# Kernel tuning notes

Measured on AMD Instinct MI355X. Metric: run time of the kernel, lower is better.

## Reference

```python
import jax, jax.numpy as jnp
import numpy as np

B, S, D = 4, 4096, 64

def setup_inputs() -> dict:
    key = jax.random.key(0)
    kq, kk, kv = jax.random.split(key, 3)
    return {
        "q": jax.random.normal(kq, (B, S, D), dtype=jnp.float32),
        "k": jax.random.normal(kk, (B, S, D), dtype=jnp.float32),
        "v": jax.random.normal(kv, (B, S, D), dtype=jnp.float32),
    }

def reference(q, k, v):
    # scores: [B, Sq, Sk]; NOTE: scale is k.shape[-1] (not sqrt), per the source.
    scores = jnp.einsum("bqd,bkd->bqk", q, k) / k.shape[-1]
    # softmax over dim=1 == the QUERY axis (non-standard), then matmul V.
    probs = jax.nn.softmax(scores, axis=1)            # [B, Sq, Sk]
    attn = jnp.einsum("bqk,bkd->bqd", probs, v)       # [B, Sq, D]
    attn_w = jax.nn.softmax(attn, axis=1)             # softmax over Sq again
    return (attn, attn_w)
```

## Files before the change

### kernel.cpp

```cpp
#include <hip/hip_runtime.h>
#include <hip/hip_bf16.h>
#include <math.h>

#define BB 4
#define SS 4096
#define DD 64
#define KSPLIT 4
#define QSPLIT 8

typedef __attribute__((ext_vector_type(8))) short short8;
typedef __attribute__((ext_vector_type(4))) float f32x4;
typedef __attribute__((ext_vector_type(2))) unsigned int u32x2;
typedef unsigned int u32;
typedef unsigned short ushort_t;

#define MFMA16(a,b,c) __builtin_amdgcn_mfma_f32_16x16x32_bf16((a),(b),(c),0,0,0)
#define C2SC 0.022542110700140054f

#define BAR() do { asm volatile("" ::: "memory"); \
                   __builtin_amdgcn_s_barrier();  \
                   asm volatile("" ::: "memory"); } while (0)
#define WAIT_VM(N)  asm volatile("s_waitcnt vmcnt(" #N ")" ::: "memory")
#define WAIT_LGKM() asm volatile("s_waitcnt lgkmcnt(0)" ::: "memory")

union Pk8 { short8 s8; u32 u[4]; u32x2 h[2]; };

static __device__ __forceinline__ unsigned short f2bf(float f) {
  union { float f; u32 u; } x; x.f = f;
  u32 r = (x.u + 0x7FFFu + ((x.u >> 16) & 1u)) >> 16;
  return (unsigned short)r;
}

static __device__ __forceinline__ u32 pk2(float a, float b) {
  __hip_bfloat16 lo = __float2bfloat16(a);
  __hip_bfloat16 hi = __float2bfloat16(b);
  unsigned short ls, hs;
  __builtin_memcpy(&ls, &lo, 2); __builtin_memcpy(&hs, &hi, 2);
  return (u32)ls | ((u32)hs << 16);
}

static __device__ __forceinline__ void gload16(const void* g, void* l) {
  __builtin_amdgcn_global_load_lds((const __attribute__((address_space(1))) u32*)g,
                                   (__attribute__((address_space(3))) u32*)l, 16, 0, 0);
}

__global__ __launch_bounds__(256) void p0_convert(
    const float* __restrict__ q, const float* __restrict__ k,
    ushort_t* __restrict__ QB, ushort_t* __restrict__ KB,
    float* __restrict__ out0, float* __restrict__ z2)
{
  const size_t i = (size_t)blockIdx.x * 256 + threadIdx.x;
  float4 a = ((const float4*)q)[i];
  float4 c = ((const float4*)k)[i];
  ((ushort4*)QB)[i] = make_ushort4(f2bf(a.x), f2bf(a.y), f2bf(a.z), f2bf(a.w));
  ((ushort4*)KB)[i] = make_ushort4(f2bf(c.x), f2bf(c.y), f2bf(c.z), f2bf(c.w));
  ((float4*)out0)[i] = make_float4(0.f, 0.f, 0.f, 0.f);
  if (blockIdx.x == 0) z2[threadIdx.x] = 0.f;
}

__global__ __launch_bounds__(256, 4) void pa_colsum(
    const ushort_t* __restrict__ QB, const ushort_t* __restrict__ KB,
    float* __restrict__ Zp)
{
  const int kb0 = blockIdx.x * 128;
  const int qch = blockIdx.y;
  const int b   = blockIdx.z;
  const int t = threadIdx.x, w = t >> 6, lane = t & 63;
  const int g = lane >> 4, r15 = lane & 15;
  const int QCH = SS / QSPLIT;
  const int NT = QCH / 64;

  __shared__ alignas(16) char qbuf[2][64*128];

  short8 ak[2][2];
#pragma unroll
  for (int s = 0; s < 2; ++s)
#pragma unroll
    for (int dh = 0; dh < 2; ++dh)
      ak[s][dh] = *(const short8*)(KB + ((size_t)b*SS + kb0 + 32*w + 16*s + r15)*DD + 32*dh + 8*g);

  const int q0g = qch * QCH;
#define PA_STAGE(tt, buf) do {                                              \
    _Pragma("unroll")                                                       \
    for (int j = 0; j < 2; ++j) {                                           \
      const int row = 16*w + 8*j + (lane >> 3);                             \
      const char* gsrc = (const char*)(QB + ((size_t)b*SS + q0g + (tt)*64 + row)*DD) \
                         + 16*((lane & 7) ^ (row & 7));                     \
      gload16(gsrc, qbuf[buf] + (16*w + 8*j)*128);                          \
    }                                                                       \
  } while (0)

  PA_STAGE(0, 0);

  float z[8];
#pragma unroll
  for (int i = 0; i < 8; ++i) z[i] = 0.f;

#pragma unroll 1
  for (int tt = 0; tt < NT; ++tt) {
    if (tt < NT-1) {
      PA_STAGE(tt+1, (tt+1)&1);
      WAIT_VM(2);
    } else {
      WAIT_VM(0);
    }
    BAR();
    const char* qb = qbuf[tt & 1];
#pragma unroll
    for (int qt = 0; qt < 4; ++qt) {
      const int qrow = 16*qt + r15;
      const char* base = qb + qrow*128;
      short8 bq0 = *(const short8*)(base + 16*((g    ) ^ (qrow & 7)));
      short8 bq1 = *(const short8*)(base + 16*((4 + g) ^ (qrow & 7)));
#pragma unroll
      for (int s = 0; s < 2; ++s) {
        f32x4 a = {0.f,0.f,0.f,0.f};
        a = MFMA16(ak[s][0], bq0, a);
        a = MFMA16(ak[s][1], bq1, a);
        z[4*s+0] += exp2f(a[0]*C2SC); z[4*s+1] += exp2f(a[1]*C2SC);
        z[4*s+2] += exp2f(a[2]*C2SC); z[4*s+3] += exp2f(a[3]*C2SC);
      }
    }
    WAIT_LGKM();
    BAR();
  }
#undef PA_STAGE

#pragma unroll
  for (int m = 1; m < 16; m <<= 1)
#pragma unroll
    for (int i = 0; i < 8; ++i) z[i] += __shfl_xor(z[i], m);
  if (r15 == 0) {
#pragma unroll
    for (int s = 0; s < 2; ++s)
#pragma unroll
      for (int r = 0; r < 4; ++r)
        Zp[((size_t)qch*BB + b)*SS + kb0 + 32*w + 16*s + 4*g + r] = z[4*s+r];
  }
}

__global__ __launch_bounds__(256) void p2_vt(
    const float* __restrict__ v, const float* __restrict__ Zp,
    ushort_t* __restrict__ VT)
{
  const int k0 = blockIdx.x * 64;
  const int b  = blockIdx.y;
  const int t = threadIdx.x;
  __shared__ float vs[64][65];
  __shared__ float izs[64];
  {
    const int row = t >> 2, cq = (t & 3) * 16;
    const float* src = v + ((size_t)b*SS + k0 + row)*DD + cq;
#pragma unroll
    for (int i = 0; i < 4; ++i) {
      float4 x = ((const float4*)src)[i];
      vs[row][cq + 4*i + 0] = x.x; vs[row][cq + 4*i + 1] = x.y;
      vs[row][cq + 4*i + 2] = x.z; vs[row][cq + 4*i + 3] = x.w;
    }
  }
  if (t < 64) {
    float z = 0.f;
#pragma unroll
    for (int c = 0; c < QSPLIT; ++c)
      z += Zp[((size_t)c*BB + b)*SS + k0 + t];
    izs[t] = 1.0f / z;
  }
  __syncthreads();
  const int d = t >> 2, ks = (t & 3) * 16;
  u32* dst = (u32*)VT + (((size_t)b*DD + d)*SS + k0 + ks)/2;
#pragma unroll
  for (int i = 0; i < 8; ++i) {
    float a0 = vs[ks + 2*i    ][d] * izs[ks + 2*i    ];
    float a1 = vs[ks + 2*i + 1][d] * izs[ks + 2*i + 1];
    dst[i] = (u32)f2bf(a0) | ((u32)f2bf(a1) << 16);
  }
}

__global__ __launch_bounds__(256, 2) void pb_attn(
    const ushort_t* __restrict__ QB, const ushort_t* __restrict__ KB,
    const ushort_t* __restrict__ VT, float* __restrict__ out0)
{
  const int q0 = blockIdx.x * 64;
  const int kbase = blockIdx.y * (SS / KSPLIT);
  const int b  = blockIdx.z;
  const int t = threadIdx.x, w = t >> 6, lane = t & 63;
  const int g = lane >> 4, r15 = lane & 15;
  const int NT = SS / KSPLIT / 128;

  __shared__ alignas(16) char smem[65536];
  char* kbuf = smem;
  char* vbuf = smem + 32768;

  short8 aq[4][2];
#pragma unroll
  for (int qt = 0; qt < 4; ++qt)
#pragma unroll
    for (int dh = 0; dh < 2; ++dh)
      aq[qt][dh] = *(const short8*)(QB + ((size_t)b*SS + q0 + 16*qt + r15)*DD + 32*dh + 8*g);

  f32x4 acc[4][4];
#pragma unroll
  for (int qt = 0; qt < 4; ++qt)
#pragma unroll
    for (int dt = 0; dt < 4; ++dt) acc[qt][dt] = (f32x4){0.f,0.f,0.f,0.f};

#define PB_STAGE(kt, buf) do {                                               \
    const int kc = kbase + (kt)*128;                                         \
    _Pragma("unroll")                                                        \
    for (int j = 0; j < 4; ++j) {                                            \
      const int row = 32*j + 8*w + (lane >> 3);                              \
      const char* gk = (const char*)(KB + ((size_t)b*SS + kc + row)*DD)      \
                       + 16*((lane & 7) ^ (row & 7));                        \
      gload16(gk, kbuf + (buf)*16384 + (32*j + 8*w)*128);                    \
    }                                                                        \
    _Pragma("unroll")                                                        \
    for (int j = 0; j < 4; ++j) {                                            \
      const int row = 16*j + 4*w + (lane >> 4);                              \
      const char* gv = (const char*)(VT + ((size_t)b*DD + row)*SS + kc)      \
                       + 16*((lane & 15) ^ (row & 15));                      \
      gload16(gv, vbuf + (buf)*16384 + (16*j + 4*w)*256);                    \
    }                                                                        \
  } while (0)

  PB_STAGE(0, 0);

#pragma unroll 1
  for (int kt = 0; kt < NT; ++kt) {
    if (kt < NT-1) {
      PB_STAGE(kt+1, (kt+1)&1);
      WAIT_VM(8);
    } else {
      WAIT_VM(0);
    }
    BAR();
    const char* kb = kbuf + (kt&1)*16384;
    const char* vb = vbuf + (kt&1)*16384;

    u32 pk[2][4][2];
#pragma unroll
    for (int s = 0; s < 2; ++s) {
      const int rowA = 64*s + 16*w + r15;
      const char* base = kb + rowA*128;
      short8 ka0 = *(const short8*)(base + 16*((g    ) ^ (rowA & 7)));
      short8 ka1 = *(const short8*)(base + 16*((4 + g) ^ (rowA & 7)));
#pragma unroll
      for (int qt = 0; qt < 4; ++qt) {
        f32x4 a = {0.f,0.f,0.f,0.f};
        a = MFMA16(ka0, aq[qt][0], a);
        a = MFMA16(ka1, aq[qt][1], a);
        pk[s][qt][0] = pk2(exp2f(a[0]*C2SC), exp2f(a[1]*C2SC));
        pk[s][qt][1] = pk2(exp2f(a[2]*C2SC), exp2f(a[3]*C2SC));
      }
    }
    short8 bv[4];
#pragma unroll
    for (int dt = 0; dt < 4; ++dt) {
      const int vrow = 16*dt + r15;
      Pk8 u;
      u.h[0] = *(const u32x2*)(vb + vrow*256 + 16*((    2*w + (g>>1)) ^ r15) + 8*(g&1));
      u.h[1] = *(const u32x2*)(vb + vrow*256 + 16*((8 + 2*w + (g>>1)) ^ r15) + 8*(g&1));
      bv[dt] = u.s8;
    }
#pragma unroll
    for (int qt = 0; qt < 4; ++qt) {
      Pk8 ap;
      ap.u[0] = pk[0][qt][0]; ap.u[1] = pk[0][qt][1];
      ap.u[2] = pk[1][qt][0]; ap.u[3] = pk[1][qt][1];
#pragma unroll
      for (int dt = 0; dt < 4; ++dt)
        acc[qt][dt] = MFMA16(ap.s8, bv[dt], acc[qt][dt]);
    }
    WAIT_LGKM();
    BAR();
  }
#undef PB_STAGE

  f32x4* red = (f32x4*)smem;
  if (w > 0) {
#pragma unroll
    for (int qt = 0; qt < 4; ++qt)
#pragma unroll
      for (int dt = 0; dt < 4; ++dt) red[((w-1)*16 + qt*4+dt)*64 + lane] = acc[qt][dt];
  }
  __syncthreads();
  if (w == 0) {
#pragma unroll
    for (int qt = 0; qt < 4; ++qt)
#pragma unroll
      for (int dt = 0; dt < 4; ++dt) {
        f32x4 s = acc[qt][dt] + red[(0*16 + qt*4+dt)*64 + lane]
                + red[(1*16 + qt*4+dt)*64 + lane] + red[(2*16 + qt*4+dt)*64 + lane];
#pragma unroll
        for (int rr = 0; rr < 4; ++rr)
          atomicAdd(&out0[((size_t)b*SS + q0 + 16*qt + 4*g + rr)*DD + 16*dt + r15], s[rr]);
      }
  }
}

__global__ __launch_bounds__(256) void k4f(
    const float* __restrict__ attn, float* __restrict__ z2)
{
  const int b = blockIdx.x;
  const int q0 = blockIdx.y * 32;
  const int t = threadIdx.x;
  const int d = t & 63, rg = t >> 6;
  float ze = 0.f;
#pragma unroll
  for (int i = 0; i < 8; ++i) {
    float a = attn[((size_t)b*SS + q0 + 4*i + rg)*DD + d];
    ze += __expf(a);
  }
  __shared__ float red[4][64];
  red[rg][d] = ze;
  __syncthreads();
  if (t < 64)
    atomicAdd(&z2[b*DD + t], red[0][t] + red[1][t] + red[2][t] + red[3][t]);
}

__global__ __launch_bounds__(256) void k6w(
    const float* __restrict__ attn, const float* __restrict__ z2,
    float* __restrict__ out1)
{
  const size_t i = (size_t)blockIdx.x * 256 + threadIdx.x;
  const int b = (int)(i >> 18);
  const int d = (int)(i & 63);
  out1[i] = __expf(attn[i]) / z2[b*DD + d];
}

extern "C" void kernel_launch(void* const* d_in, const int* in_sizes, int n_in,
                              void* d_out, int out_size, void* d_ws, size_t ws_size,
                              hipStream_t stream) {
  const float* q = (const float*)d_in[0];
  const float* k = (const float*)d_in[1];
  const float* v = (const float*)d_in[2];
  float* out0 = (float*)d_out;
  float* out1 = out0 + (size_t)BB * SS * DD;

  ushort_t* QB = (ushort_t*)out1;
  ushort_t* KB = QB + (size_t)BB * SS * DD;

  float* ws = (float*)d_ws;
  ushort_t* VT = (ushort_t*)ws;
  float* Zp = (float*)(VT + (size_t)BB * DD * SS);
  float* z2 = Zp + (size_t)QSPLIT * BB * SS;

  hipLaunchKernelGGL(p0_convert, dim3(BB*SS*DD/4/256), dim3(256), 0, stream, q, k, QB, KB, out0, z2);
  hipLaunchKernelGGL(pa_colsum, dim3(SS/128, QSPLIT, BB), dim3(256), 0, stream, QB, KB, Zp);
  hipLaunchKernelGGL(p2_vt, dim3(SS/64, BB), dim3(256), 0, stream, v, Zp, VT);
  hipLaunchKernelGGL(pb_attn, dim3(SS/64, KSPLIT, BB), dim3(256), 0, stream, QB, KB, VT, out0);
  hipLaunchKernelGGL(k4f, dim3(BB, SS/32), dim3(256), 0, stream, out0, z2);
  hipLaunchKernelGGL(k6w, dim3(BB*SS*DD/256), dim3(256), 0, stream, out0, z2, out1);
}
```

Measured before the change: 85.96 us.

## Widen attention blocks to 512 threads and replace atomics with split-K partial buffers

The attention kernel now uses 512-thread blocks covering 128 queries, with two 4-wave groups sharing each K/V tile load. That halves the global loads per thread, and the cross-wave reduction becomes a two-step tree. When workspace allows, each K-split writes its partial output to a separate buffer, and a new combine kernel sums them and computes the column exp-sums, replacing the float atomics. The column-sum kernel also doubles its query split, raises its occupancy hint, and drops the explicit LDS waitcnt. The partial buffers add extra memory traffic and depend on workspace size.

```diff
diff --git a/kernel.cpp b/kernel.cpp
--- a/kernel.cpp
+++ b/kernel.cpp
@@ -6,7 +6,7 @@
 #define SS 4096
 #define DD 64
 #define KSPLIT 4
-#define QSPLIT 8
+#define QSPLIT 16
 
 typedef __attribute__((ext_vector_type(8))) short short8;
 typedef __attribute__((ext_vector_type(4))) float f32x4;
@@ -21,7 +21,6 @@
                    __builtin_amdgcn_s_barrier();  \
                    asm volatile("" ::: "memory"); } while (0)
 #define WAIT_VM(N)  asm volatile("s_waitcnt vmcnt(" #N ")" ::: "memory")
-#define WAIT_LGKM() asm volatile("s_waitcnt lgkmcnt(0)" ::: "memory")
 
 union Pk8 { short8 s8; u32 u[4]; u32x2 h[2]; };
 
@@ -58,7 +57,7 @@
   if (blockIdx.x == 0) z2[threadIdx.x] = 0.f;
 }
 
-__global__ __launch_bounds__(256, 4) void pa_colsum(
+__global__ __launch_bounds__(256, 6) void pa_colsum(
     const ushort_t* __restrict__ QB, const ushort_t* __restrict__ KB,
     float* __restrict__ Zp)
 {
@@ -121,7 +120,6 @@
         z[4*s+2] += exp2f(a[2]*C2SC); z[4*s+3] += exp2f(a[3]*C2SC);
       }
     }
-    WAIT_LGKM();
     BAR();
   }
 #undef PA_STAGE
@@ -176,15 +174,19 @@
   }
 }
 
-__global__ __launch_bounds__(256, 2) void pb_attn(
+template<int MODE>
+__global__ __launch_bounds__(512, 4) void pb_attn(
     const ushort_t* __restrict__ QB, const ushort_t* __restrict__ KB,
-    const ushort_t* __restrict__ VT, float* __restrict__ out0)
-{
-  const int q0 = blockIdx.x * 64;
-  const int kbase = blockIdx.y * (SS / KSPLIT);
+    const ushort_t* __restrict__ VT, float* __restrict__ outp)
+{
+  const int q0 = blockIdx.x * 128;
+  const int ky = blockIdx.y;
+  const int kbase = ky * (SS / KSPLIT);
   const int b  = blockIdx.z;
-  const int t = threadIdx.x, w = t >> 6, lane = t & 63;
+  const int t = threadIdx.x, w8 = t >> 6, lane = t & 63;
+  const int w = w8 & 3, h = w8 >> 2;
   const int g = lane >> 4, r15 = lane & 15;
+  const int qbase = q0 + 64*h;
   const int NT = SS / KSPLIT / 128;
 
   __shared__ alignas(16) char smem[65536];
@@ -196,7 +198,7 @@
   for (int qt = 0; qt < 4; ++qt)
 #pragma unroll
     for (int dh = 0; dh < 2; ++dh)
-      aq[qt][dh] = *(const short8*)(QB + ((size_t)b*SS + q0 + 16*qt + r15)*DD + 32*dh + 8*g);
+      aq[qt][dh] = *(const short8*)(QB + ((size_t)b*SS + qbase + 16*qt + r15)*DD + 32*dh + 8*g);
 
   f32x4 acc[4][4];
 #pragma unroll
@@ -207,18 +209,18 @@
 #define PB_STAGE(kt, buf) do {                                               \
     const int kc = kbase + (kt)*128;                                         \
     _Pragma("unroll")                                                        \
-    for (int j = 0; j < 4; ++j) {                                            \
-      const int row = 32*j + 8*w + (lane >> 3);                              \
+    for (int j = 0; j < 2; ++j) {                                            \
+      const int row = 16*w8 + 8*j + (lane >> 3);                             \
       const char* gk = (const char*)(KB + ((size_t)b*SS + kc + row)*DD)      \
                        + 16*((lane & 7) ^ (row & 7));                        \
-      gload16(gk, kbuf + (buf)*16384 + (32*j + 8*w)*128);                    \
+      gload16(gk, kbuf + (buf)*16384 + (16*w8 + 8*j)*128);                   \
     }                                                                        \
     _Pragma("unroll")                                                        \
-    for (int j = 0; j < 4; ++j) {                                            \
-      const int row = 16*j + 4*w + (lane >> 4);                              \
+    for (int j = 0; j < 2; ++j) {                                            \
+      const int row = 8*w8 + 4*j + (lane >> 4);                              \
       const char* gv = (const char*)(VT + ((size_t)b*DD + row)*SS + kc)      \
                        + 16*((lane & 15) ^ (row & 15));                      \
-      gload16(gv, vbuf + (buf)*16384 + (16*j + 4*w)*256);                    \
+      gload16(gv, vbuf + (buf)*16384 + (8*w8 + 4*j)*256);                    \
     }                                                                        \
   } while (0)
 
@@ -228,7 +230,7 @@
   for (int kt = 0; kt < NT; ++kt) {
     if (kt < NT-1) {
       PB_STAGE(kt+1, (kt+1)&1);
-      WAIT_VM(8);
+      WAIT_VM(4);
     } else {
       WAIT_VM(0);
     }
@@ -270,29 +272,57 @@
       for (int dt = 0; dt < 4; ++dt)
         acc[qt][dt] = MFMA16(ap.s8, bv[dt], acc[qt][dt]);
     }
-    WAIT_LGKM();
     BAR();
   }
 #undef PB_STAGE
 
-  f32x4* red = (f32x4*)smem;
-  if (w > 0) {
-#pragma unroll
-    for (int qt = 0; qt < 4; ++qt)
-#pragma unroll
-      for (int dt = 0; dt < 4; ++dt) red[((w-1)*16 + qt*4+dt)*64 + lane] = acc[qt][dt];
+  f32x4* red = (f32x4*)(smem + h*32768);
+  if (w == 1) {
+#pragma unroll
+    for (int qt = 0; qt < 4; ++qt)
+#pragma unroll
+      for (int dt = 0; dt < 4; ++dt) red[(qt*4+dt)*64 + lane] = acc[qt][dt];
+  }
+  if (w == 3) {
+#pragma unroll
+    for (int qt = 0; qt < 4; ++qt)
+#pragma unroll
+      for (int dt = 0; dt < 4; ++dt) red[1024 + (qt*4+dt)*64 + lane] = acc[qt][dt];
   }
   __syncthreads();
   if (w == 0) {
 #pragma unroll
     for (int qt = 0; qt < 4; ++qt)
 #pragma unroll
+      for (int dt = 0; dt < 4; ++dt) acc[qt][dt] += red[(qt*4+dt)*64 + lane];
+  }
+  if (w == 2) {
+#pragma unroll
+    for (int qt = 0; qt < 4; ++qt)
+#pragma unroll
+      for (int dt = 0; dt < 4; ++dt) acc[qt][dt] += red[1024 + (qt*4+dt)*64 + lane];
+  }
+  __syncthreads();
+  if (w == 2) {
+#pragma unroll
+    for (int qt = 0; qt < 4; ++qt)
+#pragma unroll
+      for (int dt = 0; dt < 4; ++dt) red[(qt*4+dt)*64 + lane] = acc[qt][dt];
+  }
+  __syncthreads();
+  if (w == 0) {
+    float* dst = (MODE == 0) ? outp : outp + (size_t)ky * BB * SS * DD;
+#pragma unroll
+    for (int qt = 0; qt < 4; ++qt)
+#pragma unroll
       for (int dt = 0; dt < 4; ++dt) {
-        f32x4 s = acc[qt][dt] + red[(0*16 + qt*4+dt)*64 + lane]
-                + red[(1*16 + qt*4+dt)*64 + lane] + red[(2*16 + qt*4+dt)*64 + lane];
-#pragma unroll
-        for (int rr = 0; rr < 4; ++rr)
-          atomicAdd(&out0[((size_t)b*SS + q0 + 16*qt + 4*g + rr)*DD + 16*dt + r15], s[rr]);
+        f32x4 s = acc[qt][dt] + red[(qt*4+dt)*64 + lane];
+#pragma unroll
+        for (int rr = 0; rr < 4; ++rr) {
+          const size_t idx = ((size_t)b*SS + qbase + 16*qt + 4*g + rr)*DD + 16*dt + r15;
+          if (MODE == 0) atomicAdd(&outp[idx], s[rr]);
+          else           dst[idx] = s[rr];
+        }
       }
   }
 }
@@ -308,6 +338,29 @@
 #pragma unroll
   for (int i = 0; i < 8; ++i) {
     float a = attn[((size_t)b*SS + q0 + 4*i + rg)*DD + d];
+    ze += __expf(a);
+  }
+  __shared__ float red[4][64];
+  red[rg][d] = ze;
+  __syncthreads();
+  if (t < 64)
+    atomicAdd(&z2[b*DD + t], red[0][t] + red[1][t] + red[2][t] + red[3][t]);
+}
+
+__global__ __launch_bounds__(256) void k5_comb(
+    const float* __restrict__ parts, float* __restrict__ out0, float* __restrict__ z2)
+{
+  const int b = blockIdx.x;
+  const int q0 = blockIdx.y * 32;
+  const int t = threadIdx.x;
+  const int d = t & 63, rg = t >> 6;
+  const size_t N = (size_t)BB * SS * DD;
+  float ze = 0.f;
+#pragma unroll
+  for (int i = 0; i < 8; ++i) {
+    const size_t idx = ((size_t)b*SS + q0 + 4*i + rg)*DD + d;
+    float a = parts[idx] + parts[N + idx] + parts[2*N + idx] + parts[3*N + idx];
+    out0[idx] = a;
     ze += __expf(a);
   }
   __shared__ float red[4][64];
@@ -339,15 +392,25 @@
   ushort_t* QB = (ushort_t*)out1;
   ushort_t* KB = QB + (size_t)BB * SS * DD;
 
-  float* ws = (float*)d_ws;
+  char* ws = (char*)d_ws;
   ushort_t* VT = (ushort_t*)ws;
-  float* Zp = (float*)(VT + (size_t)BB * DD * SS);
+  float* Zp = (float*)(ws + (size_t)BB*DD*SS*2);
   float* z2 = Zp + (size_t)QSPLIT * BB * SS;
+  float* parts = z2 + 256;
+
+  const size_t need = (size_t)BB*DD*SS*2 + (size_t)QSPLIT*BB*SS*4 + 1024
+                    + (size_t)KSPLIT*BB*SS*DD*4;
+  const bool use_parts = (ws_size >= need);
 
   hipLaunchKernelGGL(p0_convert, dim3(BB*SS*DD/4/256), dim3(256), 0, stream, q, k, QB, KB, out0, z2);
   hipLaunchKernelGGL(pa_colsum, dim3(SS/128, QSPLIT, BB), dim3(256), 0, stream, QB, KB, Zp);
   hipLaunchKernelGGL(p2_vt, dim3(SS/64, BB), dim3(256), 0, stream, v, Zp, VT);
-  hipLaunchKernelGGL(pb_attn, dim3(SS/64, KSPLIT, BB), dim3(256), 0, stream, QB, KB, VT, out0);
-  hipLaunchKernelGGL(k4f, dim3(BB, SS/32), dim3(256), 0, stream, out0, z2);
+  if (use_parts) {
+    pb_attn<1><<<dim3(SS/128, KSPLIT, BB), dim3(512), 0, stream>>>(QB, KB, VT, parts);
+    hipLaunchKernelGGL(k5_comb, dim3(BB, SS/32), dim3(256), 0, stream, parts, out0, z2);
+  } else {
+    pb_attn<0><<<dim3(SS/128, KSPLIT, BB), dim3(512), 0, stream>>>(QB, KB, VT, out0);
+    hipLaunchKernelGGL(k4f, dim3(BB, SS/32), dim3(256), 0, stream, out0, z2);
+  }
   hipLaunchKernelGGL(k6w, dim3(BB*SS*DD/256), dim3(256), 0, stream, out0, z2, out1);
 }
```

After: 134.2 us. 1.56x slower.
